# Optimization experiments

Hardware: AMD Instinct MI355X
Metric: run time of the kernel (lower is better)

Reference implementation:

```python
import jax, jax.numpy as jnp
import numpy as np
import math

S, N, L = 4, 10000, 8
IN, H = 64, 64
D = IN + 2 * H + 1  # rnn input: feats + bidirectional walk enc + degree


def _gru(x, h0, Wih, Whh, bih, bhh, reverse=False):
    """Torch-semantics GRU. x: (B, L, Din), h0: (B, H). Gate order r,z,n."""
    xw = jnp.einsum('bld,gd->blg', x, Wih) + bih  # precompute input proj (B,L,3H)

    def step(h, xw_t):
        gh = h @ Whh.T + bhh
        xr, xz, xn = jnp.split(xw_t, 3, axis=-1)
        hr, hz, hn = jnp.split(gh, 3, axis=-1)
        r = jax.nn.sigmoid(xr + hr)
        z = jax.nn.sigmoid(xz + hz)
        n = jnp.tanh(xn + r * hn)
        h = (1.0 - z) * n + z * h
        return h, h

    hT, ys = jax.lax.scan(step, h0, jnp.swapaxes(xw, 0, 1), reverse=reverse)
    return jnp.swapaxes(ys, 0, 1), hT  # (B,L,H), (B,H)


def setup_inputs() -> dict:
    key = jax.random.key(0)
    ks = jax.random.split(key, 16)
    w = lambda k, shape: (jax.random.normal(k, shape, jnp.float32) * 0.1)
    inp = {
        'h': jax.random.normal(ks[0], (N, IN), jnp.float32),
        'walks': jax.random.randint(ks[1], (S, N, L), 0, N, dtype=jnp.int32),
        'in_degrees': jax.random.randint(ks[2], (N,), 1, 50, dtype=jnp.int32),
        # bidirectional walk GRU (input=2)
        'Wih_f': w(ks[3], (3 * H, 2)), 'Whh_f': w(ks[4], (3 * H, H)),
        'bih_f': w(ks[5], (3 * H,)), 'bhh_f': w(ks[6], (3 * H,)),
        'Wih_b': w(ks[7], (3 * H, 2)), 'Whh_b': w(ks[8], (3 * H, H)),
        'bih_b': w(ks[9], (3 * H,)), 'bhh_b': w(ks[10], (3 * H,)),
        # main GRU (input=D)
        'Wih': w(ks[11], (3 * H, D)), 'Whh': w(ks[12], (3 * H, H)),
        'bih': w(ks[13], (3 * H,)), 'bhh': w(ks[14], (3 * H,)),
    }
    return inp


def reference(h, walks, in_degrees, Wih_f, Whh_f, bih_f, bhh_f,
              Wih_b, Whh_b, bih_b, bhh_b, Wih, Whh, bih, bhh):
    S_, N_, L_ = walks.shape
    # uniqueness: first-occurrence index of each node within its walk
    eq = walks[..., :, None] == walks[..., None, :]          # (S,N,L,L)
    u = jnp.argmax(eq, axis=-1).astype(h.dtype)              # (S,N,L)
    walks = walks[..., ::-1]
    u = u[..., ::-1]
    u = (u / L_) * (2.0 * math.pi)
    uw = jnp.stack([jnp.sin(u), jnp.cos(u)], axis=-1)        # (S,N,L,2)

    hw = h[walks]                                            # gather (S,N,L,IN)
    deg = in_degrees.astype(h.dtype)[walks][..., None]       # (S,N,L,1)
    deg = deg / deg.max()

    B = S_ * N_
    uw2 = uw.reshape(B, L_, 2)
    h0 = jnp.zeros((B, H), h.dtype)
    yf, hf = _gru(uw2, h0, Wih_f, Whh_f, bih_f, bhh_f)
    yb, hb = _gru(uw2, h0, Wih_b, Whh_b, bih_b, bhh_b, reverse=True)
    y_walk = jnp.concatenate([yf, yb], axis=-1).reshape(S_, N_, L_, 2 * H)
    h_walk = 0.5 * (hf + hb)                                 # mean over directions (B,H)

    x = jnp.concatenate([hw, y_walk, deg], axis=-1).reshape(B, L_, D)
    _, hT = _gru(x, h_walk, Wih, Whh, bih, bhh)
    # final hidden has layer dim of size 1; .mean(0) is identity -> (S,N,H)
    out = hT.reshape(S_, N_, H)
    return out
```

## Files before the change

kernel.cpp:

```cpp
#include <hip/hip_runtime.h>
#include <hip/hip_bf16.h>

#define NN   10000
#define SS   4
#define BB   40000
#define LLEN 8
#define DD   193
#define G3   192

typedef __attribute__((ext_vector_type(8))) short bf16x8;
typedef __attribute__((ext_vector_type(4))) short short4v;
typedef __attribute__((ext_vector_type(4))) float f32x4;

#define OFF_DMAX 0
#define OFF_DEGN 1024
#define OFF_A    65536
#define OFF_YF   (8ull*1024*1024)
#define OFF_YB   (49ull*1024*1024)
#define OFF_HFB  (90ull*1024*1024)

__device__ __forceinline__ float sigm(float x){ return 1.0f/(1.0f+__expf(-x)); }
__device__ __forceinline__ float tanh_(float x){
  float e = __expf(-2.0f*fabsf(x));
  float t = (1.0f-e)/(1.0f+e);
  return x>=0.0f ? t : -t;
}
__device__ __forceinline__ short f2b(float f){
  unsigned u = __builtin_bit_cast(unsigned, f);
  u = u + 0x7FFFu + ((u>>16)&1u);
  return (short)(u>>16);
}
__device__ __forceinline__ float b2f(short s){
  unsigned u = ((unsigned)(unsigned short)s)<<16;
  return __builtin_bit_cast(float, u);
}

__global__ void k_zero(int* dmax){
  if (threadIdx.x==0 && blockIdx.x==0) *dmax = 0;
}

__global__ void k_degmax(const int* __restrict__ walks, const int* __restrict__ indeg,
                         int* __restrict__ dmax){
  int i = blockIdx.x*blockDim.x + threadIdx.x;
  int d = 0;
  if (i < SS*NN*LLEN) d = indeg[walks[i]];
  #pragma unroll
  for (int off=32; off>0; off>>=1) d = max(d, __shfl_xor(d, off));
  if ((threadIdx.x&63)==0 && d>0) atomicMax(dmax, d);
}

__global__ void k_degn(const int* __restrict__ indeg, const int* __restrict__ dmax,
                       float* __restrict__ degn){
  int n = blockIdx.x*blockDim.x + threadIdx.x;
  if (n < NN) degn[n] = (float)indeg[n] / (float)(*dmax);
}

__global__ __launch_bounds__(192) void k_A(const float* __restrict__ h,
                                           const float* __restrict__ Wih,
                                           const float* __restrict__ bih,
                                           float* __restrict__ A){
  int g = threadIdx.x;
  float w[64];
  #pragma unroll
  for (int k=0;k<64;++k) w[k] = Wih[g*DD + k];
  float bg = bih[g];
  __shared__ float hs[64];
  int n0 = blockIdx.x*32;
  for (int j=0;j<32;++j){
    int n = n0 + j;
    if (n >= NN) break;
    __syncthreads();
    if (g < 64) hs[g] = h[n*64+g];
    __syncthreads();
    float acc = bg;
    #pragma unroll
    for (int k=0;k<64;++k) acc += w[k]*hs[k];
    A[n*G3 + g] = acc;
  }
}

__global__ __launch_bounds__(256,3) void k_fb(
    const int* __restrict__ walks,
    const float* __restrict__ Wih_f, const float* __restrict__ Whh_f,
    const float* __restrict__ bih_f, const float* __restrict__ bhh_f,
    const float* __restrict__ Wih_b, const float* __restrict__ Whh_b,
    const float* __restrict__ bih_b, const float* __restrict__ bhh_b,
    short* __restrict__ yf_out, short* __restrict__ yb_out,
    short* __restrict__ hfb)
{
  const int dir = blockIdx.y;
  const float* Wih = dir ? Wih_b : Wih_f;
  const float* Whh = dir ? Whh_b : Whh_f;
  const float* bih = dir ? bih_b : bih_f;
  const float* bhh = dir ? bhh_b : bhh_f;
  short* yout = dir ? yb_out : yf_out;

  __shared__ __align__(16) short Wlds[192*64];
  __shared__ __align__(16) short A2[192*8];
  __shared__ __align__(16) short hl[64*64];
  __shared__ __align__(16) float sc[64*8*2];
  __shared__ __align__(16) float bhn[64];

  const int tid = threadIdx.x;
  const int b0  = blockIdx.x*64;

  for (int idx = tid; idx < 192*64; idx += 256){
    int g = idx>>6, k = idx&63;
    Wlds[g*64 + (k ^ ((g&7)<<3))] = f2b(Whh[idx]);
  }
  for (int g = tid; g < 192; g += 256){
    A2[g*8+0] = f2b(Wih[2*g]);
    A2[g*8+1] = f2b(Wih[2*g+1]);
    float bb = bih[g] + (g < 128 ? bhh[g] : 0.0f);
    A2[g*8+2] = f2b(bb);
    A2[g*8+3]=0; A2[g*8+4]=0; A2[g*8+5]=0; A2[g*8+6]=0; A2[g*8+7]=0;
  }
  if (tid < 64) bhn[tid] = bhh[128+tid];
  for (int idx = tid; idx < 512; idx += 256){
    int s = idx>>3, t = idx&7, p = 7-t;
    const int* wr = walks + (long)(b0+s)*LLEN;
    int wp = wr[p]; int u = 7;
    #pragma unroll
    for (int j=7;j>=0;--j) if (wr[j]==wp) u = j;
    float si, ci;
    __sincosf((float)u * 0.7853981633974483f, &si, &ci);
    sc[idx*2] = si; sc[idx*2+1] = ci;
  }
  __syncthreads();

  const int lane = tid & 63;
  const int wv   = tid >> 6;
  const int c    = lane & 15;
  const int a    = lane >> 4;
  const int s    = wv*16 + c;
  const int sg   = b0 + s;

  float hreg[4][4];
  short4v z4 = {0,0,0,0};
  #pragma unroll
  for (int q=0;q<4;++q){
    #pragma unroll
    for (int r=0;r<4;++r) hreg[q][r] = 0.0f;
    int i0 = q*16 + 4*a;
    *(short4v*)&hl[s*64 + (i0 ^ ((s&7)<<3))] = z4;
  }

  for (int ss=0; ss<8; ++ss){
    const int t = dir ? 7-ss : ss;
    asm volatile("s_waitcnt lgkmcnt(0)" ::: "memory");
    bf16x8 bh0 = *(const bf16x8*)&hl[s*64 + ((a*8)      ^ ((s&7)<<3))];
    bf16x8 bh1 = *(const bf16x8*)&hl[s*64 + ((32 + a*8) ^ ((s&7)<<3))];
    bf16x8 b2 = {0,0,0,0,0,0,0,0};
    if (a == 0){
      b2[0] = f2b(sc[(s*8+t)*2]);
      b2[1] = f2b(sc[(s*8+t)*2+1]);
      b2[2] = (short)0x3F80;
    }
    f32x4 acc1[12]; f32x4 acc2[4];
    #pragma unroll
    for (int T=0;T<12;++T){ acc1[T].x=0;acc1[T].y=0;acc1[T].z=0;acc1[T].w=0; }
    #pragma unroll
    for (int T=0;T<4;++T){ acc2[T].x=0;acc2[T].y=0;acc2[T].z=0;acc2[T].w=0; }

    #pragma unroll
    for (int T=0;T<12;++T){
      int g = 16*T + c;
      bf16x8 a0 = *(const bf16x8*)&Wlds[g*64 + ((a*8)      ^ ((g&7)<<3))];
      bf16x8 a1 = *(const bf16x8*)&Wlds[g*64 + ((32 + a*8) ^ ((g&7)<<3))];
      acc1[T] = __builtin_amdgcn_mfma_f32_16x16x32_bf16(a0, bh0, acc1[T], 0,0,0);
      acc1[T] = __builtin_amdgcn_mfma_f32_16x16x32_bf16(a1, bh1, acc1[T], 0,0,0);
      bf16x8 a2 = *(const bf16x8*)&A2[g*8];
      if (T < 8) acc1[T]   = __builtin_amdgcn_mfma_f32_16x16x32_bf16(a2, b2, acc1[T],   0,0,0);
      else       acc2[T-8] = __builtin_amdgcn_mfma_f32_16x16x32_bf16(a2, b2, acc2[T-8], 0,0,0);
    }

    #pragma unroll
    for (int q=0;q<4;++q){
      int i0 = q*16 + 4*a;
      f32x4 bv = *(const f32x4*)&bhn[i0];
      short4v pack;
      #pragma unroll
      for (int r=0;r<4;++r){
        float rr = sigm(acc1[q][r]);
        float zz = sigm(acc1[4+q][r]);
        float hn = acc1[8+q][r] + bv[r];
        float xn = acc2[q][r];
        float nn = tanh_(xn + rr*hn);
        float hv = (1.0f-zz)*nn + zz*hreg[q][r];
        hreg[q][r] = hv;
        pack[r] = f2b(hv);
      }
      *(short4v*)&hl[s*64 + (i0 ^ ((s&7)<<3))] = pack;
      int kb = 4*q + a;
      *(short4v*)(yout + ((long)(t*16+kb)*BB + sg)*4) = pack;
    }
  }

  #pragma unroll
  for (int q=0;q<4;++q){
    int i0 = q*16 + 4*a;
    short4v pk;
    #pragma unroll
    for (int r=0;r<4;++r) pk[r] = f2b(hreg[q][r]);
    *(short4v*)(hfb + ((long)dir*BB + sg)*64 + i0) = pk;
  }
}

__global__ __launch_bounds__(256,1) void k_final(
    const int* __restrict__ walks, const float* __restrict__ degn,
    const float* __restrict__ A,
    const float* __restrict__ W, const float* __restrict__ U,
    const float* __restrict__ bhh,
    const short* __restrict__ yf, const short* __restrict__ yb,
    const short* __restrict__ hfb,
    float* __restrict__ out)
{
  __shared__ __align__(16) short Ulds[192*64];
  __shared__ __align__(16) short Wy[192*128];
  __shared__ __align__(16) short A5[192*8];
  __shared__ __align__(16) short hl[64*64];
  __shared__ __align__(16) int   node[64*8];
  __shared__ __align__(16) float degl[64*8];
  __shared__ __align__(16) float bhn[64];

  const int tid = threadIdx.x;
  const int b0  = blockIdx.x*64;

  for (int idx = tid; idx < 192*64; idx += 256){
    int g = idx>>6, k = idx&63;
    Ulds[g*64 + (k ^ ((g&7)<<3))] = f2b(U[idx]);
  }
  for (int idx = tid; idx < 192*128; idx += 256){
    int g = idx>>7, k2 = idx&127;
    Wy[g*128 + (k2 ^ ((g&7)<<3))] = f2b(W[(long)g*DD + 64 + k2]);
  }
  for (int g = tid; g < 192; g += 256){
    A5[g*8+0] = f2b(W[(long)g*DD + 192]);
    A5[g*8+1] = (g < 128) ? f2b(bhh[g]) : (short)0;
    A5[g*8+2]=0; A5[g*8+3]=0; A5[g*8+4]=0; A5[g*8+5]=0; A5[g*8+6]=0; A5[g*8+7]=0;
  }
  if (tid < 64) bhn[tid] = bhh[128+tid];
  for (int idx = tid; idx < 512; idx += 256){
    int s = idx>>3, t = idx&7;
    int nd = walks[(long)(b0+s)*LLEN + 7-t];
    node[idx] = nd;
    degl[idx] = degn[nd];
  }
  __syncthreads();

  const int lane = tid & 63;
  const int wv   = tid >> 6;
  const int c    = lane & 15;
  const int a    = lane >> 4;
  const int s    = wv*16 + c;
  const int sg   = b0 + s;

  float hreg[4][4];
  #pragma unroll
  for (int q=0;q<4;++q){
    int i0 = q*16 + 4*a;
    short4v hf4 = *(const short4v*)(hfb + (long)sg*64 + i0);
    short4v hb4 = *(const short4v*)(hfb + ((long)BB + sg)*64 + i0);
    short4v pk;
    #pragma unroll
    for (int r=0;r<4;++r){
      float hv = 0.5f*(b2f(hf4[r]) + b2f(hb4[r]));
      hreg[q][r] = hv;
      pk[r] = f2b(hv);
    }
    *(short4v*)&hl[s*64 + (i0 ^ ((s&7)<<3))] = pk;
  }

  auto ldy = [&](const short* Y, int t, int kh, bf16x8& dst){
    int ky0 = kh*32 + a*8;
    int kb  = ky0 >> 2;
    long base = ((long)(t*16 + kb)*BB + sg)*4;
    short4v lo = *(const short4v*)(Y + base);
    short4v hi = *(const short4v*)(Y + base + (long)BB*4);
    dst[0]=lo[0]; dst[1]=lo[1]; dst[2]=lo[2]; dst[3]=lo[3];
    dst[4]=hi[0]; dst[5]=hi[1]; dst[6]=hi[2]; dst[7]=hi[3];
  };

  bf16x8 yfc[2], ybc[2];
  ldy(yf, 0, 0, yfc[0]); ldy(yf, 0, 1, yfc[1]);
  ldy(yb, 0, 0, ybc[0]); ldy(yb, 0, 1, ybc[1]);

  for (int t=0; t<8; ++t){
    bf16x8 yfn[2], ybn[2];
    if (t < 7){
      ldy(yf, t+1, 0, yfn[0]); ldy(yf, t+1, 1, yfn[1]);
      ldy(yb, t+1, 0, ybn[0]); ldy(yb, t+1, 1, ybn[1]);
    }
    int nd = node[s*8 + t];
    f32x4 Ag[12];
    #pragma unroll
    for (int T=0;T<12;++T) Ag[T] = *(const f32x4*)(A + (long)nd*192 + 16*T + 4*a);

    asm volatile("s_waitcnt lgkmcnt(0)" ::: "memory");
    bf16x8 bh0 = *(const bf16x8*)&hl[s*64 + ((a*8)      ^ ((s&7)<<3))];
    bf16x8 bh1 = *(const bf16x8*)&hl[s*64 + ((32 + a*8) ^ ((s&7)<<3))];
    bf16x8 b5 = {0,0,0,0,0,0,0,0};
    if (a == 0){
      b5[0] = f2b(degl[s*8+t]);
      b5[1] = (short)0x3F80;
    }

    f32x4 acc1[12]; f32x4 acc2[4];
    #pragma unroll
    for (int T=0;T<12;++T){ acc1[T].x=0;acc1[T].y=0;acc1[T].z=0;acc1[T].w=0; }
    #pragma unroll
    for (int T=0;T<4;++T){ acc2[T].x=0;acc2[T].y=0;acc2[T].z=0;acc2[T].w=0; }

    #pragma unroll
    for (int T=0;T<12;++T){
      int g = 16*T + c;
      bf16x8 u0 = *(const bf16x8*)&Ulds[g*64 + ((a*8)      ^ ((g&7)<<3))];
      bf16x8 u1 = *(const bf16x8*)&Ulds[g*64 + ((32 + a*8) ^ ((g&7)<<3))];
      acc1[T] = __builtin_amdgcn_mfma_f32_16x16x32_bf16(u0, bh0, acc1[T], 0,0,0);
      acc1[T] = __builtin_amdgcn_mfma_f32_16x16x32_bf16(u1, bh1, acc1[T], 0,0,0);
      bf16x8 w0 = *(const bf16x8*)&Wy[g*128 + ((a*8)       ^ ((g&7)<<3))];
      bf16x8 w1 = *(const bf16x8*)&Wy[g*128 + ((32 + a*8)  ^ ((g&7)<<3))];
      bf16x8 w2 = *(const bf16x8*)&Wy[g*128 + ((64 + a*8)  ^ ((g&7)<<3))];
      bf16x8 w3 = *(const bf16x8*)&Wy[g*128 + ((96 + a*8)  ^ ((g&7)<<3))];
      bf16x8 a5 = *(const bf16x8*)&A5[g*8];
      if (T < 8){
        acc1[T] = __builtin_amdgcn_mfma_f32_16x16x32_bf16(w0, yfc[0], acc1[T], 0,0,0);
        acc1[T] = __builtin_amdgcn_mfma_f32_16x16x32_bf16(w1, yfc[1], acc1[T], 0,0,0);
        acc1[T] = __builtin_amdgcn_mfma_f32_16x16x32_bf16(w2, ybc[0], acc1[T], 0,0,0);
        acc1[T] = __builtin_amdgcn_mfma_f32_16x16x32_bf16(w3, ybc[1], acc1[T], 0,0,0);
        acc1[T] = __builtin_amdgcn_mfma_f32_16x16x32_bf16(a5, b5,     acc1[T], 0,0,0);
      } else {
        acc2[T-8] = __builtin_amdgcn_mfma_f32_16x16x32_bf16(w0, yfc[0], acc2[T-8], 0,0,0);
        acc2[T-8] = __builtin_amdgcn_mfma_f32_16x16x32_bf16(w1, yfc[1], acc2[T-8], 0,0,0);
        acc2[T-8] = __builtin_amdgcn_mfma_f32_16x16x32_bf16(w2, ybc[0], acc2[T-8], 0,0,0);
        acc2[T-8] = __builtin_amdgcn_mfma_f32_16x16x32_bf16(w3, ybc[1], acc2[T-8], 0,0,0);
        acc2[T-8] = __builtin_amdgcn_mfma_f32_16x16x32_bf16(a5, b5,     acc2[T-8], 0,0,0);
      }
    }

    #pragma unroll
    for (int q=0;q<4;++q){
      int i0 = q*16 + 4*a;
      f32x4 bv = *(const f32x4*)&bhn[i0];
      short4v pack;
      #pragma unroll
      for (int r=0;r<4;++r){
        float rr = sigm(acc1[q][r]   + Ag[q][r]);
        float zz = sigm(acc1[4+q][r] + Ag[4+q][r]);
        float hn = acc1[8+q][r] + bv[r];
        float xn = acc2[q][r]   + Ag[8+q][r];
        float nn = tanh_(xn + rr*hn);
        float hv = (1.0f-zz)*nn + zz*hreg[q][r];
        hreg[q][r] = hv;
        pack[r] = f2b(hv);
      }
      *(short4v*)&hl[s*64 + (i0 ^ ((s&7)<<3))] = pack;
    }

    if (t < 7){
      yfc[0]=yfn[0]; yfc[1]=yfn[1];
      ybc[0]=ybn[0]; ybc[1]=ybn[1];
    }
  }

  #pragma unroll
  for (int q=0;q<4;++q){
    int i0 = q*16 + 4*a;
    f32x4 o;
    #pragma unroll
    for (int r=0;r<4;++r) o[r] = hreg[q][r];
    *(f32x4*)(out + (long)sg*64 + i0) = o;
  }
}

extern "C" void kernel_launch(void* const* d_in, const int* in_sizes, int n_in,
                              void* d_out, int out_size, void* d_ws, size_t ws_size,
                              hipStream_t stream) {
  const float* h     = (const float*)d_in[0];
  const int*   walks = (const int*)d_in[1];
  const int*   indeg = (const int*)d_in[2];
  const float* Wf    = (const float*)d_in[3];
  const float* Uf    = (const float*)d_in[4];
  const float* bif   = (const float*)d_in[5];
  const float* bhf   = (const float*)d_in[6];
  const float* Wb    = (const float*)d_in[7];
  const float* Ub    = (const float*)d_in[8];
  const float* bib   = (const float*)d_in[9];
  const float* bhb   = (const float*)d_in[10];
  const float* W     = (const float*)d_in[11];
  const float* U     = (const float*)d_in[12];
  const float* bi    = (const float*)d_in[13];
  const float* bh    = (const float*)d_in[14];
  float* out = (float*)d_out;

  char* ws = (char*)d_ws;
  int*   dmax = (int*)(ws + OFF_DMAX);
  float* degn = (float*)(ws + OFF_DEGN);
  float* A    = (float*)(ws + OFF_A);
  short* yfw  = (short*)(ws + OFF_YF);
  short* ybw  = (short*)(ws + OFF_YB);
  short* hfb  = (short*)(ws + OFF_HFB);

  k_zero<<<1, 64, 0, stream>>>(dmax);
  k_degmax<<<(SS*NN*LLEN + 255)/256, 256, 0, stream>>>(walks, indeg, dmax);
  k_degn<<<(NN + 255)/256, 256, 0, stream>>>(indeg, dmax, degn);
  k_A<<<(NN + 31)/32, 192, 0, stream>>>(h, W, bi, A);
  k_fb<<<dim3(BB/64, 2), 256, 0, stream>>>(walks,
                                           Wf, Uf, bif, bhf,
                                           Wb, Ub, bib, bhb,
                                           yfw, ybw, hfb);
  k_final<<<BB/64, 256, 0, stream>>>(walks, degn, A, W, U, bh,
                                     yfw, ybw, hfb, out);
}
```

Before: 383.5 us.

## Fuse bidirectional walk GRU and main GRU into one kernel with register-held outputs

```diff
diff --git a/kernel.cpp b/kernel.cpp
--- a/kernel.cpp
+++ b/kernel.cpp
@@ -7,6 +7,8 @@
 #define LLEN 8
 #define DD   193
 #define G3   192
+#define SPB  128
+#define THREADS 512
 
 typedef __attribute__((ext_vector_type(8))) short bf16x8;
 typedef __attribute__((ext_vector_type(4))) short short4v;
@@ -14,10 +16,7 @@
 
 #define OFF_DMAX 0
 #define OFF_DEGN 1024
-#define OFF_A    65536
-#define OFF_YF   (8ull*1024*1024)
-#define OFF_YB   (49ull*1024*1024)
-#define OFF_HFB  (90ull*1024*1024)
+#define OFF_A    262144
 
 __device__ __forceinline__ float sigm(float x){ return 1.0f/(1.0f+__expf(-x)); }
 __device__ __forceinline__ float tanh_(float x){
@@ -79,53 +78,91 @@
   }
 }
 
-__global__ __launch_bounds__(256,3) void k_fb(
-    const int* __restrict__ walks,
-    const float* __restrict__ Wih_f, const float* __restrict__ Whh_f,
+__global__ __launch_bounds__(THREADS, 2) void k_fused(
+    const int* __restrict__ walks, const float* __restrict__ degn,
+    const float* __restrict__ A,
+    const float* __restrict__ Whh_f, const float* __restrict__ Wih_f,
     const float* __restrict__ bih_f, const float* __restrict__ bhh_f,
-    const float* __restrict__ Wih_b, const float* __restrict__ Whh_b,
+    const float* __restrict__ Whh_b, const float* __restrict__ Wih_b,
     const float* __restrict__ bih_b, const float* __restrict__ bhh_b,
-    short* __restrict__ yf_out, short* __restrict__ yb_out,
-    short* __restrict__ hfb)
+    const float* __restrict__ W, const float* __restrict__ U,
+    const float* __restrict__ bhh,
+    float* __restrict__ out)
 {
-  const int dir = blockIdx.y;
-  const float* Wih = dir ? Wih_b : Wih_f;
-  const float* Whh = dir ? Whh_b : Whh_f;
-  const float* bih = dir ? bih_b : bih_f;
-  const float* bhh = dir ? bhh_b : bhh_f;
-  short* yout = dir ? yb_out : yf_out;
-
-  __shared__ __align__(16) short Wlds[192*64];
-  __shared__ __align__(16) short A2[192*8];
-  __shared__ __align__(16) short hl[64*64];
-  __shared__ __align__(16) float sc[64*8*2];
+  __shared__ __align__(16) short WL[84*512];
+  __shared__ __align__(16) short hl[SPB*64];
+  __shared__ __align__(16) float sc[SPB*8*2];
+  __shared__ __align__(16) int   node[SPB*8];
+  __shared__ __align__(16) float degl[SPB*8];
   __shared__ __align__(16) float bhn[64];
 
   const int tid = threadIdx.x;
-  const int b0  = blockIdx.x*64;
-
-  for (int idx = tid; idx < 192*64; idx += 256){
-    int g = idx>>6, k = idx&63;
-    Wlds[g*64 + (k ^ ((g&7)<<3))] = f2b(Whh[idx]);
-  }
-  for (int g = tid; g < 192; g += 256){
-    A2[g*8+0] = f2b(Wih[2*g]);
-    A2[g*8+1] = f2b(Wih[2*g+1]);
-    float bb = bih[g] + (g < 128 ? bhh[g] : 0.0f);
-    A2[g*8+2] = f2b(bb);
-    A2[g*8+3]=0; A2[g*8+4]=0; A2[g*8+5]=0; A2[g*8+6]=0; A2[g*8+7]=0;
-  }
-  if (tid < 64) bhn[tid] = bhh[128+tid];
-  for (int idx = tid; idx < 512; idx += 256){
+  const int b0  = blockIdx.x*SPB;
+
+  for (int idx = tid; idx < SPB*8; idx += THREADS){
     int s = idx>>3, t = idx&7, p = 7-t;
-    const int* wr = walks + (long)(b0+s)*LLEN;
+    long bsg = b0 + s; if (bsg >= BB) bsg = BB-1;
+    const int* wr = walks + bsg*LLEN;
     int wp = wr[p]; int u = 7;
     #pragma unroll
     for (int j=7;j>=0;--j) if (wr[j]==wp) u = j;
     float si, ci;
     __sincosf((float)u * 0.7853981633974483f, &si, &ci);
     sc[idx*2] = si; sc[idx*2+1] = ci;
-  }
+    node[idx] = wp;
+    degl[idx] = degn[wp];
+  }
+
+  auto stage_fb = [&](const float* Whh, const float* Wih,
+                      const float* bih, const float* bhd){
+    for (int sl = tid; sl < 36*64; sl += THREADS){
+      int f = sl>>6, ln = sl&63;
+      int ch = f%3, gt = (f/3)%3, q = f/9;
+      int g = gt*64 + q*16 + (ln&15);
+      int kb = (ln>>4)*8;
+      short v[8];
+      if (ch < 2){
+        #pragma unroll
+        for (int j=0;j<8;++j) v[j] = f2b(Whh[g*64 + ch*32 + kb + j]);
+      } else {
+        #pragma unroll
+        for (int j=0;j<8;++j){
+          int kk = kb + j;
+          v[j] = (kk==0) ? f2b(Wih[2*g]) : (kk==1) ? f2b(Wih[2*g+1])
+               : (kk==2) ? f2b(bih[g] + (g<128 ? bhd[g] : 0.0f)) : (short)0;
+        }
+      }
+      *(bf16x8*)&WL[sl*8] = *(bf16x8*)v;
+    }
+    if (tid < 64) bhn[tid] = bhd[128+tid];
+  };
+  auto stage_final = [&](){
+    for (int sl = tid; sl < 84*64; sl += THREADS){
+      int f = sl>>6, ln = sl&63;
+      int ch = f%7, gt = (f/7)%3, q = f/21;
+      int g = gt*64 + q*16 + (ln&15);
+      int kb = (ln>>4)*8;
+      short v[8];
+      if (ch < 2){
+        #pragma unroll
+        for (int j=0;j<8;++j) v[j] = f2b(U[g*64 + ch*32 + kb + j]);
+      } else if (ch < 6){
+        #pragma unroll
+        for (int j=0;j<8;++j) v[j] = f2b(W[(long)g*DD + 64 + (ch-2)*32 + kb + j]);
+      } else {
+        #pragma unroll
+        for (int j=0;j<8;++j){
+          int kk = kb + j;
+          v[j] = (kk==0) ? f2b(W[(long)g*DD + 192])
+               : (kk==1) ? f2b(g<128 ? bhh[g] : 0.0f) : (short)0;
+        }
+      }
+      *(bf16x8*)&WL[sl*8] = *(bf16x8*)v;
+    }
+    if (tid < 64) bhn[tid] = bhh[128+tid];
+  };
+
+  stage_fb(Whh_f, Wih_f, bih_f, bhh_f);
   __syncthreads();
 
   const int lane = tid & 63;
@@ -133,244 +170,155 @@
   const int c    = lane & 15;
   const int a    = lane >> 4;
   const int s    = wv*16 + c;
-  const int sg   = b0 + s;
-
+  const long sg  = b0 + s;
+  const int swz  = (s&7)<<3;
+
+  const bf16x8 zf = {0,0,0,0,0,0,0,0};
   float hreg[4][4];
-  short4v z4 = {0,0,0,0};
-  #pragma unroll
-  for (int q=0;q<4;++q){
+  bf16x8 bh0 = zf, bh1 = zf;
+  bf16x8 yfr0[8], yfr1[8], ybr0[8], ybr1[8];
+
+  #pragma unroll
+  for (int q=0;q<4;++q)
     #pragma unroll
     for (int r=0;r<4;++r) hreg[q][r] = 0.0f;
-    int i0 = q*16 + 4*a;
-    *(short4v*)&hl[s*64 + (i0 ^ ((s&7)<<3))] = z4;
-  }
-
+
+#define GRU_FB_STEP(t)                                                          \
+  {                                                                             \
+    bf16x8 b2 = zf;                                                             \
+    if (a == 0){                                                                \
+      b2[0] = f2b(sc[(s*8+(t))*2]); b2[1] = f2b(sc[(s*8+(t))*2+1]);             \
+      b2[2] = (short)0x3F80;                                                    \
+    }                                                                           \
+    _Pragma("unroll")                                                           \
+    for (int q=0;q<4;++q){                                                      \
+      f32x4 ar = {0,0,0,0}, az = {0,0,0,0}, an1 = {0,0,0,0}, an2 = {0,0,0,0};   \
+      _Pragma("unroll")                                                         \
+      for (int ch=0; ch<3; ++ch){                                               \
+        bf16x8 fr = *(const bf16x8*)&WL[(((q*3+0)*3+ch)<<9) + lane*8];          \
+        bf16x8 fz = *(const bf16x8*)&WL[(((q*3+1)*3+ch)<<9) + lane*8];          \
+        bf16x8 fn = *(const bf16x8*)&WL[(((q*3+2)*3+ch)<<9) + lane*8];          \
+        bf16x8 bb = (ch==0) ? bh0 : (ch==1) ? bh1 : b2;                         \
+        ar = __builtin_amdgcn_mfma_f32_16x16x32_bf16(fr, bb, ar, 0,0,0);        \
+        az = __builtin_amdgcn_mfma_f32_16x16x32_bf16(fz, bb, az, 0,0,0);        \
+        if (ch < 2) an1 = __builtin_amdgcn_mfma_f32_16x16x32_bf16(fn, bb, an1, 0,0,0); \
+        else        an2 = __builtin_amdgcn_mfma_f32_16x16x32_bf16(fn, bb, an2, 0,0,0); \
+      }                                                                         \
+      f32x4 bv = *(const f32x4*)&bhn[q*16 + 4*a];                               \
+      short4v pack;                                                             \
+      _Pragma("unroll")                                                         \
+      for (int r=0;r<4;++r){                                                    \
+        float rr = sigm(ar[r]);                                                 \
+        float zz = sigm(az[r]);                                                 \
+        float nn = tanh_(an2[r] + rr*(an1[r] + bv[r]));                         \
+        float hv = (1.0f-zz)*nn + zz*hreg[q][r];                                \
+        hreg[q][r] = hv;                                                        \
+        pack[r] = f2b(hv);                                                      \
+      }                                                                         \
+      *(short4v*)&hl[s*64 + ((q*16 + 4*a) ^ swz)] = pack;                       \
+    }                                                                           \
+    bh0 = *(const bf16x8*)&hl[s*64 + ((a*8)      ^ swz)];                       \
+    bh1 = *(const bf16x8*)&hl[s*64 + ((32 + a*8) ^ swz)];                       \
+  }
+
+  #pragma unroll
   for (int ss=0; ss<8; ++ss){
-    const int t = dir ? 7-ss : ss;
-    asm volatile("s_waitcnt lgkmcnt(0)" ::: "memory");
-    bf16x8 bh0 = *(const bf16x8*)&hl[s*64 + ((a*8)      ^ ((s&7)<<3))];
-    bf16x8 bh1 = *(const bf16x8*)&hl[s*64 + ((32 + a*8) ^ ((s&7)<<3))];
-    bf16x8 b2 = {0,0,0,0,0,0,0,0};
-    if (a == 0){
-      b2[0] = f2b(sc[(s*8+t)*2]);
-      b2[1] = f2b(sc[(s*8+t)*2+1]);
-      b2[2] = (short)0x3F80;
-    }
-    f32x4 acc1[12]; f32x4 acc2[4];
-    #pragma unroll
-    for (int T=0;T<12;++T){ acc1[T].x=0;acc1[T].y=0;acc1[T].z=0;acc1[T].w=0; }
-    #pragma unroll
-    for (int T=0;T<4;++T){ acc2[T].x=0;acc2[T].y=0;acc2[T].z=0;acc2[T].w=0; }
-
-    #pragma unroll
-    for (int T=0;T<12;++T){
-      int g = 16*T + c;
-      bf16x8 a0 = *(const bf16x8*)&Wlds[g*64 + ((a*8)      ^ ((g&7)<<3))];
-      bf16x8 a1 = *(const bf16x8*)&Wlds[g*64 + ((32 + a*8) ^ ((g&7)<<3))];
-      acc1[T] = __builtin_amdgcn_mfma_f32_16x16x32_bf16(a0, bh0, acc1[T], 0,0,0);
-      acc1[T] = __builtin_amdgcn_mfma_f32_16x16x32_bf16(a1, bh1, acc1[T], 0,0,0);
-      bf16x8 a2 = *(const bf16x8*)&A2[g*8];
-      if (T < 8) acc1[T]   = __builtin_amdgcn_mfma_f32_16x16x32_bf16(a2, b2, acc1[T],   0,0,0);
-      else       acc2[T-8] = __builtin_amdgcn_mfma_f32_16x16x32_bf16(a2, b2, acc2[T-8], 0,0,0);
-    }
-
+    GRU_FB_STEP(ss)
+    yfr0[ss] = bh0; yfr1[ss] = bh1;
+  }
+  __syncthreads();
+  stage_fb(Whh_b, Wih_b, bih_b, bhh_b);
+  __syncthreads();
+
+  bh0 = zf; bh1 = zf;
+  #pragma unroll
+  for (int q=0;q<4;++q)
+    #pragma unroll
+    for (int r=0;r<4;++r) hreg[q][r] = 0.0f;
+  #pragma unroll
+  for (int ss=0; ss<8; ++ss){
+    const int t = 7-ss;
+    GRU_FB_STEP(t)
+    ybr0[t] = bh0; ybr1[t] = bh1;
+  }
+  __syncthreads();
+  stage_final();
+  __syncthreads();
+
+  {
+    bf16x8 hw0, hw1;
+    #pragma unroll
+    for (int j=0;j<8;++j){
+      hw0[j] = f2b(0.5f*(b2f(yfr0[7][j]) + b2f(ybr0[0][j])));
+      hw1[j] = f2b(0.5f*(b2f(yfr1[7][j]) + b2f(ybr1[0][j])));
+    }
+    *(bf16x8*)&hl[s*64 + ((a*8)      ^ swz)] = hw0;
+    *(bf16x8*)&hl[s*64 + ((32 + a*8) ^ swz)] = hw1;
+    bh0 = hw0; bh1 = hw1;
     #pragma unroll
     for (int q=0;q<4;++q){
-      int i0 = q*16 + 4*a;
-      f32x4 bv = *(const f32x4*)&bhn[i0];
+      short4v h4 = *(const short4v*)&hl[s*64 + ((q*16 + 4*a) ^ swz)];
+      #pragma unroll
+      for (int r=0;r<4;++r) hreg[q][r] = b2f(h4[r]);
+    }
+  }
+
+  #pragma unroll
+  for (int t=0; t<8; ++t){
+    bf16x8 b5 = zf;
+    if (a == 0){ b5[0] = f2b(degl[s*8+t]); b5[1] = (short)0x3F80; }
+    const int nd = node[s*8+t];
+    const bf16x8 yy0 = yfr0[t], yy1 = yfr1[t], yy2 = ybr0[t], yy3 = ybr1[t];
+
+    #pragma unroll
+    for (int q=0;q<4;++q){
+      f32x4 ar = {0,0,0,0}, az = {0,0,0,0}, an1 = {0,0,0,0}, an2 = {0,0,0,0};
+      #pragma unroll
+      for (int ch=0; ch<7; ++ch){
+        bf16x8 fr = *(const bf16x8*)&WL[(((q*3+0)*7+ch)<<9) + lane*8];
+        bf16x8 fz = *(const bf16x8*)&WL[(((q*3+1)*7+ch)<<9) + lane*8];
+        bf16x8 fn = *(const bf16x8*)&WL[(((q*3+2)*7+ch)<<9) + lane*8];
+        bf16x8 bb = (ch==0) ? bh0 : (ch==1) ? bh1
+                  : (ch==2) ? yy0 : (ch==3) ? yy1
+                  : (ch==4) ? yy2 : (ch==5) ? yy3 : b5;
+        ar = __builtin_amdgcn_mfma_f32_16x16x32_bf16(fr, bb, ar, 0,0,0);
+        az = __builtin_amdgcn_mfma_f32_16x16x32_bf16(fz, bb, az, 0,0,0);
+        if (ch < 2) an1 = __builtin_amdgcn_mfma_f32_16x16x32_bf16(fn, bb, an1, 0,0,0);
+        else        an2 = __builtin_amdgcn_mfma_f32_16x16x32_bf16(fn, bb, an2, 0,0,0);
+      }
+      const float* Ab = A + (long)nd*G3 + q*16 + 4*a;
+      f32x4 Agr = *(const f32x4*)(Ab);
+      f32x4 Agz = *(const f32x4*)(Ab + 64);
+      f32x4 Agn = *(const f32x4*)(Ab + 128);
+      f32x4 bv  = *(const f32x4*)&bhn[q*16 + 4*a];
       short4v pack;
       #pragma unroll
       for (int r=0;r<4;++r){
-        float rr = sigm(acc1[q][r]);
-        float zz = sigm(acc1[4+q][r]);
-        float hn = acc1[8+q][r] + bv[r];
-        float xn = acc2[q][r];
-        float nn = tanh_(xn + rr*hn);
+        float rr = sigm(ar[r] + Agr[r]);
+        float zz = sigm(az[r] + Agz[r]);
+        float nn = tanh_(an2[r] + Agn[r] + rr*(an1[r] + bv[r]));
         float hv = (1.0f-zz)*nn + zz*hreg[q][r];
         hreg[q][r] = hv;
         pack[r] = f2b(hv);
       }
-      *(short4v*)&hl[s*64 + (i0 ^ ((s&7)<<3))] = pack;
-      int kb = 4*q + a;
-      *(short4v*)(yout + ((long)(t*16+kb)*BB + sg)*4) = pack;
-    }
-  }
-
-  #pragma unroll
-  for (int q=0;q<4;++q){
-    int i0 = q*16 + 4*a;
-    short4v pk;
-    #pragma unroll
-    for (int r=0;r<4;++r) pk[r] = f2b(hreg[q][r]);
-    *(short4v*)(hfb + ((long)dir*BB + sg)*64 + i0) = pk;
-  }
-}
-
-__global__ __launch_bounds__(256,1) void k_final(
-    const int* __restrict__ walks, const float* __restrict__ degn,
-    const float* __restrict__ A,
-    const float* __restrict__ W, const float* __restrict__ U,
-    const float* __restrict__ bhh,
-    const short* __restrict__ yf, const short* __restrict__ yb,
-    const short* __restrict__ hfb,
-    float* __restrict__ out)
-{
-  __shared__ __align__(16) short Ulds[192*64];
-  __shared__ __align__(16) short Wy[192*128];
-  __shared__ __align__(16) short A5[192*8];
-  __shared__ __align__(16) short hl[64*64];
-  __shared__ __align__(16) int   node[64*8];
-  __shared__ __align__(16) float degl[64*8];
-  __shared__ __align__(16) float bhn[64];
-
-  const int tid = threadIdx.x;
-  const int b0  = blockIdx.x*64;
-
-  for (int idx = tid; idx < 192*64; idx += 256){
-    int g = idx>>6, k = idx&63;
-    Ulds[g*64 + (k ^ ((g&7)<<3))] = f2b(U[idx]);
-  }
-  for (int idx = tid; idx < 192*128; idx += 256){
-    int g = idx>>7, k2 = idx&127;
-    Wy[g*128 + (k2 ^ ((g&7)<<3))] = f2b(W[(long)g*DD + 64 + k2]);
-  }
-  for (int g = tid; g < 192; g += 256){
-    A5[g*8+0] = f2b(W[(long)g*DD + 192]);
-    A5[g*8+1] = (g < 128) ? f2b(bhh[g]) : (short)0;
-    A5[g*8+2]=0; A5[g*8+3]=0; A5[g*8+4]=0; A5[g*8+5]=0; A5[g*8+6]=0; A5[g*8+7]=0;
-  }
-  if (tid < 64) bhn[tid] = bhh[128+tid];
-  for (int idx = tid; idx < 512; idx += 256){
-    int s = idx>>3, t = idx&7;
-    int nd = walks[(long)(b0+s)*LLEN + 7-t];
-    node[idx] = nd;
-    degl[idx] = degn[nd];
-  }
-  __syncthreads();
-
-  const int lane = tid & 63;
-  const int wv   = tid >> 6;
-  const int c    = lane & 15;
-  const int a    = lane >> 4;
-  const int s    = wv*16 + c;
-  const int sg   = b0 + s;
-
-  float hreg[4][4];
-  #pragma unroll
-  for (int q=0;q<4;++q){
-    int i0 = q*16 + 4*a;
-    short4v hf4 = *(const short4v*)(hfb + (long)sg*64 + i0);
-    short4v hb4 = *(const short4v*)(hfb + ((long)BB + sg)*64 + i0);
-    short4v pk;
-    #pragma unroll
-    for (int r=0;r<4;++r){
-      float hv = 0.5f*(b2f(hf4[r]) + b2f(hb4[r]));
-      hreg[q][r] = hv;
-      pk[r] = f2b(hv);
-    }
-    *(short4v*)&hl[s*64 + (i0 ^ ((s&7)<<3))] = pk;
-  }
-
-  auto ldy = [&](const short* Y, int t, int kh, bf16x8& dst){
-    int ky0 = kh*32 + a*8;
-    int kb  = ky0 >> 2;
-    long base = ((long)(t*16 + kb)*BB + sg)*4;
-    short4v lo = *(const short4v*)(Y + base);
-    short4v hi = *(const short4v*)(Y + base + (long)BB*4);
-    dst[0]=lo[0]; dst[1]=lo[1]; dst[2]=lo[2]; dst[3]=lo[3];
-    dst[4]=hi[0]; dst[5]=hi[1]; dst[6]=hi[2]; dst[7]=hi[3];
-  };
-
-  bf16x8 yfc[2], ybc[2];
-  ldy(yf, 0, 0, yfc[0]); ldy(yf, 0, 1, yfc[1]);
-  ldy(yb, 0, 0, ybc[0]); ldy(yb, 0, 1, ybc[1]);
-
-  for (int t=0; t<8; ++t){
-    bf16x8 yfn[2], ybn[2];
+      *(short4v*)&hl[s*64 + ((q*16 + 4*a) ^ swz)] = pack;
+    }
     if (t < 7){
-      ldy(yf, t+1, 0, yfn[0]); ldy(yf, t+1, 1, yfn[1]);
-      ldy(yb, t+1, 0, ybn[0]); ldy(yb, t+1, 1, ybn[1]);
-    }
-    int nd = node[s*8 + t];
-    f32x4 Ag[12];
-    #pragma unroll
-    for (int T=0;T<12;++T) Ag[T] = *(const f32x4*)(A + (long)nd*192 + 16*T + 4*a);
-
-    asm volatile("s_waitcnt lgkmcnt(0)" ::: "memory");
-    bf16x8 bh0 = *(const bf16x8*)&hl[s*64 + ((a*8)      ^ ((s&7)<<3))];
-    bf16x8 bh1 = *(const bf16x8*)&hl[s*64 + ((32 + a*8) ^ ((s&7)<<3))];
-    bf16x8 b5 = {0,0,0,0,0,0,0,0};
-    if (a == 0){
-      b5[0] = f2b(degl[s*8+t]);
-      b5[1] = (short)0x3F80;
-    }
-
-    f32x4 acc1[12]; f32x4 acc2[4];
-    #pragma unroll
-    for (int T=0;T<12;++T){ acc1[T].x=0;acc1[T].y=0;acc1[T].z=0;acc1[T].w=0; }
-    #pragma unroll
-    for (int T=0;T<4;++T){ acc2[T].x=0;acc2[T].y=0;acc2[T].z=0;acc2[T].w=0; }
-
-    #pragma unroll
-    for (int T=0;T<12;++T){
-      int g = 16*T + c;
-      bf16x8 u0 = *(const bf16x8*)&Ulds[g*64 + ((a*8)      ^ ((g&7)<<3))];
-      bf16x8 u1 = *(const bf16x8*)&Ulds[g*64 + ((32 + a*8) ^ ((g&7)<<3))];
-      acc1[T] = __builtin_amdgcn_mfma_f32_16x16x32_bf16(u0, bh0, acc1[T], 0,0,0);
-      acc1[T] = __builtin_amdgcn_mfma_f32_16x16x32_bf16(u1, bh1, acc1[T], 0,0,0);
-      bf16x8 w0 = *(const bf16x8*)&Wy[g*128 + ((a*8)       ^ ((g&7)<<3))];
-      bf16x8 w1 = *(const bf16x8*)&Wy[g*128 + ((32 + a*8)  ^ ((g&7)<<3))];
-      bf16x8 w2 = *(const bf16x8*)&Wy[g*128 + ((64 + a*8)  ^ ((g&7)<<3))];
-      bf16x8 w3 = *(const bf16x8*)&Wy[g*128 + ((96 + a*8)  ^ ((g&7)<<3))];
-      bf16x8 a5 = *(const bf16x8*)&A5[g*8];
-      if (T < 8){
-        acc1[T] = __builtin_amdgcn_mfma_f32_16x16x32_bf16(w0, yfc[0], acc1[T], 0,0,0);
-        acc1[T] = __builtin_amdgcn_mfma_f32_16x16x32_bf16(w1, yfc[1], acc1[T], 0,0,0);
-        acc1[T] = __builtin_amdgcn_mfma_f32_16x16x32_bf16(w2, ybc[0], acc1[T], 0,0,0);
-        acc1[T] = __builtin_amdgcn_mfma_f32_16x16x32_bf16(w3, ybc[1], acc1[T], 0,0,0);
-        acc1[T] = __builtin_amdgcn_mfma_f32_16x16x32_bf16(a5, b5,     acc1[T], 0,0,0);
-      } else {
-        acc2[T-8] = __builtin_amdgcn_mfma_f32_16x16x32_bf16(w0, yfc[0], acc2[T-8], 0,0,0);
-        acc2[T-8] = __builtin_amdgcn_mfma_f32_16x16x32_bf16(w1, yfc[1], acc2[T-8], 0,0,0);
-        acc2[T-8] = __builtin_amdgcn_mfma_f32_16x16x32_bf16(w2, ybc[0], acc2[T-8], 0,0,0);
-        acc2[T-8] = __builtin_amdgcn_mfma_f32_16x16x32_bf16(w3, ybc[1], acc2[T-8], 0,0,0);
-        acc2[T-8] = __builtin_amdgcn_mfma_f32_16x16x32_bf16(a5, b5,     acc2[T-8], 0,0,0);
-      }
-    }
-
+      bh0 = *(const bf16x8*)&hl[s*64 + ((a*8)      ^ swz)];
+      bh1 = *(const bf16x8*)&hl[s*64 + ((32 + a*8) ^ swz)];
+    }
+  }
+
+  if (sg < BB){
     #pragma unroll
     for (int q=0;q<4;++q){
-      int i0 = q*16 + 4*a;
-      f32x4 bv = *(const f32x4*)&bhn[i0];
-      short4v pack;
+      f32x4 o;
       #pragma unroll
-      for (int r=0;r<4;++r){
-        float rr = sigm(acc1[q][r]   + Ag[q][r]);
-        float zz = sigm(acc1[4+q][r] + Ag[4+q][r]);
-        float hn = acc1[8+q][r] + bv[r];
-        float xn = acc2[q][r]   + Ag[8+q][r];
-        float nn = tanh_(xn + rr*hn);
-        float hv = (1.0f-zz)*nn + zz*hreg[q][r];
-        hreg[q][r] = hv;
-        pack[r] = f2b(hv);
-      }
-      *(short4v*)&hl[s*64 + (i0 ^ ((s&7)<<3))] = pack;
-    }
-
-    if (t < 7){
-      yfc[0]=yfn[0]; yfc[1]=yfn[1];
-      ybc[0]=ybn[0]; ybc[1]=ybn[1];
-    }
-  }
-
-  #pragma unroll
-  for (int q=0;q<4;++q){
-    int i0 = q*16 + 4*a;
-    f32x4 o;
-    #pragma unroll
-    for (int r=0;r<4;++r) o[r] = hreg[q][r];
-    *(f32x4*)(out + (long)sg*64 + i0) = o;
-  }
+      for (int r=0;r<4;++r) o[r] = hreg[q][r];
+      *(f32x4*)(out + sg*64 + q*16 + 4*a) = o;
+    }
+  }
+#undef GRU_FB_STEP
 }
 
 extern "C" void kernel_launch(void* const* d_in, const int* in_sizes, int n_in,
@@ -397,18 +345,14 @@
   int*   dmax = (int*)(ws + OFF_DMAX);
   float* degn = (float*)(ws + OFF_DEGN);
   float* A    = (float*)(ws + OFF_A);
-  short* yfw  = (short*)(ws + OFF_YF);
-  short* ybw  = (short*)(ws + OFF_YB);
-  short* hfb  = (short*)(ws + OFF_HFB);
 
   k_zero<<<1, 64, 0, stream>>>(dmax);
   k_degmax<<<(SS*NN*LLEN + 255)/256, 256, 0, stream>>>(walks, indeg, dmax);
   k_degn<<<(NN + 255)/256, 256, 0, stream>>>(indeg, dmax, degn);
   k_A<<<(NN + 31)/32, 192, 0, stream>>>(h, W, bi, A);
-  k_fb<<<dim3(BB/64, 2), 256, 0, stream>>>(walks,
-                                           Wf, Uf, bif, bhf,
-                                           Wb, Ub, bib, bhb,
-                                           yfw, ybw, hfb);
-  k_final<<<BB/64, 256, 0, stream>>>(walks, degn, A, W, U, bh,
-                                     yfw, ybw, hfb, out);
-}
+  k_fused<<<(BB + SPB - 1)/SPB, THREADS, 0, stream>>>(
+      walks, degn, A,
+      Uf, Wf, bif, bhf,
+      Ub, Wb, bib, bhb,
+      W, U, bh, out);
+}
```

After: 398.7 us. 4.0% more time.
